# Kernel tuning notes

Measured on AMD Instinct MI355X. Metric: run time of the kernel, lower is better.

## Reference

```python
import jax, jax.numpy as jnp
import numpy as np


def _hungarian(cost):
    """Jonker-Volgenant shortest-augmenting-path LAP solver (minimum cost).

    Returns col_ind such that rows arange(n) are matched to columns col_ind,
    identical (in objective) to scipy.optimize.linear_sum_assignment.
    Runs on host numpy, mirroring the original's detach().cpu() + scipy path.
    """
    cost = np.asarray(cost, dtype=np.float64)
    n = cost.shape[0]
    INF = np.inf
    u = np.zeros(n + 1)
    v = np.zeros(n + 1)
    p = np.zeros(n + 1, dtype=np.int64)   # p[j]: row (1-based) assigned to column j
    way = np.zeros(n + 1, dtype=np.int64)
    for i in range(1, n + 1):
        p[0] = i
        j0 = 0
        minv = np.full(n + 1, INF)
        used = np.zeros(n + 1, dtype=bool)
        while True:
            used[j0] = True
            i0 = p[j0]
            # vectorized relaxation of reduced costs for all unused columns
            cur = cost[i0 - 1] - u[i0] - v[1:]
            free = ~used[1:]
            upd = free & (cur < minv[1:])
            minv[1:] = np.where(upd, cur, minv[1:])
            way[1:] = np.where(upd, j0, way[1:])
            cand = np.where(free, minv[1:], INF)
            j1 = int(np.argmin(cand)) + 1
            delta = cand[j1 - 1]
            u[p[used]] += delta
            v[used] -= delta
            minv[1:] = np.where(free, minv[1:] - delta, minv[1:])
            j0 = j1
            if p[j0] == 0:
                break
        # augment along the alternating path
        while j0:
            j1 = way[j0]
            p[j0] = p[j1]
            j0 = j1
    col = np.empty(n, dtype=np.int64)
    col[p[1:] - 1] = np.arange(n)
    return col


def setup_inputs() -> dict:
    key = jax.random.key(0)
    B, N = 64, 256
    D = jax.random.normal(key, (B, N, N), dtype=jnp.float32)
    return {"D": D}


def reference(D):
    # Host round-trip for the assignment, exactly as the torch module does
    # (D.detach().cpu().numpy() -> scipy LAP per batch element).
    Dn = np.asarray(jax.device_get(D))
    cols = np.stack([_hungarian(Dn[b]) for b in range(Dn.shape[0])])  # [B, N]
    idx = jnp.asarray(cols)[:, :, None]                               # [B, N, 1]
    # gather matched costs D[b, i, col[b, i]] and reduce: mean per batch, then mean
    matched = jnp.take_along_axis(D, idx, axis=2)[..., 0]             # [B, N]
    return matched.mean(axis=1).mean()
```

## Files before the change

### kernel.cpp

```cpp
#include <hip/hip_runtime.h>

#define N_DIM 256
#define BATCH 64
#define BS 64
#define SCALE 4096.0f

#define DPP_MINU(x, ctrl) do {                                                 \
    unsigned _s = (unsigned)__builtin_amdgcn_update_dpp((int)(x), (int)(x),    \
                                                        (ctrl), 0xf, 0xf, false); \
    (x) = ((x) < _s) ? (x) : _s;                                               \
} while (0)

__device__ __forceinline__ unsigned wave_min_u32(unsigned x) {
    DPP_MINU(x, 0x111);
    DPP_MINU(x, 0x112);
    DPP_MINU(x, 0x114);
    DPP_MINU(x, 0x118);
    const unsigned a = (unsigned)__builtin_amdgcn_readlane((int)x, 15);
    const unsigned b = (unsigned)__builtin_amdgcn_readlane((int)x, 31);
    const unsigned c = (unsigned)__builtin_amdgcn_readlane((int)x, 47);
    const unsigned d = (unsigned)__builtin_amdgcn_readlane((int)x, 63);
    const unsigned ab = (a < b) ? a : b;
    const unsigned cd = (c < d) ? c : d;
    return (ab < cd) ? ab : cd;
}

__device__ __forceinline__ int rd4_i(int x0, int x1, int x2, int x3, int idx) {
    const int sel = idx & 3, src = idx >> 2;
    int ab = (sel & 1) ? x1 : x0;
    int cd = (sel & 1) ? x3 : x2;
    int vv = (sel & 2) ? cd : ab;
    return __builtin_amdgcn_readlane(vv, src);
}

#define SET4(x0, x1, x2, x3, idx, val) do {                                    \
    const int _sel = (idx) & 3;                                                \
    if (t == ((idx) >> 2)) {                                                   \
        if (_sel == 0) x0 = (val); else if (_sel == 1) x1 = (val);             \
        else if (_sel == 2) x2 = (val); else x3 = (val);                       \
    }                                                                          \
} while (0)

__device__ __forceinline__ int lo16(int p) { return (int)(short)(p & 0xFFFF); }
__device__ __forceinline__ int hi16(int p) { return p >> 16; }

__global__ __launch_bounds__(BS) void lap_kernel(const float* __restrict__ Dm,
                                                 double* __restrict__ batch_sums) {
    const int b = blockIdx.x;
    const int t = threadIdx.x;
    const float* __restrict__ cost = Dm + (size_t)b * N_DIM * N_DIM;
    const float4* __restrict__ cost4 = (const float4*)cost;

    __shared__ int2     chi[N_DIM * BS];
    __shared__ int      u_s[N_DIM];
    __shared__ int      v_s[N_DIM];
    __shared__ int      row4col_s[N_DIM];
    __shared__ int      col4row_s[N_DIM];
    __shared__ int      queue_s[N_DIM];
    __shared__ unsigned bid_s[N_DIM];
    __shared__ int      qcnt_s;

    const int c0i = 4 * t, c1i = 4 * t + 1, c2i = 4 * t + 2, c3i = 4 * t + 3;

    int cmn0 = INT_MAX, cmn1 = INT_MAX, cmn2 = INT_MAX, cmn3 = INT_MAX;
    int ca0 = 0, ca1 = 0, ca2 = 0, ca3 = 0;
    for (int r = 0; r < N_DIM; ++r) {
        const float4 c4 = cost4[r * BS + t];
        const int a0 = __float2int_rn(c4.x * SCALE);
        const int a1 = __float2int_rn(c4.y * SCALE);
        const int a2 = __float2int_rn(c4.z * SCALE);
        const int a3 = __float2int_rn(c4.w * SCALE);
        int2 p;
        p.x = (a0 & 0xFFFF) | (a1 << 16);
        p.y = (a2 & 0xFFFF) | (a3 << 16);
        chi[r * BS + t] = p;
        if (a0 < cmn0) { cmn0 = a0; ca0 = r; }
        if (a1 < cmn1) { cmn1 = a1; ca1 = r; }
        if (a2 < cmn2) { cmn2 = a2; ca2 = r; }
        if (a3 < cmn3) { cmn3 = a3; ca3 = r; }
    }
    {
        int4 vv; vv.x = cmn0; vv.y = cmn1; vv.z = cmn2; vv.w = cmn3;
        ((int4*)v_s)[t] = vv;
        int4 zz; zz.x = 0; zz.y = 0; zz.z = 0; zz.w = 0;
        ((int4*)u_s)[t] = zz;
        int4 mm; mm.x = -1; mm.y = -1; mm.z = -1; mm.w = -1;
        ((int4*)row4col_s)[t] = mm;
        ((int4*)col4row_s)[t] = mm;
        int4 rc; rc.x = 0x7fffffff; rc.y = 0x7fffffff; rc.z = 0x7fffffff; rc.w = 0x7fffffff;
        ((int4*)queue_s)[t] = rc;
        uint4 bb; bb.x = ~0u; bb.y = ~0u; bb.z = ~0u; bb.w = ~0u;
        ((uint4*)bid_s)[t] = bb;
    }
    __syncthreads();
    atomicMin(&queue_s[ca0], c0i);
    atomicMin(&queue_s[ca1], c1i);
    atomicMin(&queue_s[ca2], c2i);
    atomicMin(&queue_s[ca3], c3i);
    __syncthreads();
    if (queue_s[ca0] == c0i) { row4col_s[c0i] = ca0; col4row_s[ca0] = c0i; }
    if (queue_s[ca1] == c1i) { row4col_s[c1i] = ca1; col4row_s[ca1] = c1i; }
    if (queue_s[ca2] == c2i) { row4col_s[c2i] = ca2; col4row_s[ca2] = c2i; }
    if (queue_s[ca3] == c3i) { row4col_s[c3i] = ca3; col4row_s[ca3] = c3i; }
    __syncthreads();

    for (int pass = 0; pass < 64; ++pass) {
        if (t == 0) qcnt_s = 0;
        __syncthreads();
        {
            const int4 my = ((const int4*)col4row_s)[t];
            const int nf = (my.x < 0) + (my.y < 0) + (my.z < 0) + (my.w < 0);
            if (nf) {
                int pos = atomicAdd(&qcnt_s, nf);
                if (my.x < 0) queue_s[pos++] = c0i;
                if (my.y < 0) queue_s[pos++] = c1i;
                if (my.z < 0) queue_s[pos++] = c2i;
                if (my.w < 0) queue_s[pos++] = c3i;
            }
        }
        __syncthreads();
        const int n = qcnt_s;
        if (n == 0) break;
        for (int base = 0; base < n; base += BS) {
            const int my_row = (base + t < n) ? queue_s[base + t] : -1;
            int d1 = INT_MAX, d2 = INT_MAX;
            int j1 = 0;
            if (my_row >= 0) {
                const int rb = my_row * BS;
                for (int l = 0; l < BS; ++l) {
                    const int l2 = (l + t) & 63;
                    const int2 h = chi[rb + l2];
                    const int4 vv = ((const int4*)v_s)[l2];
                    int d;
                    d = lo16(h.x) - vv.x; if (d < d1) { d2 = d1; d1 = d; j1 = 4 * l2 + 0; } else if (d < d2) d2 = d;
                    d = hi16(h.x) - vv.y; if (d < d1) { d2 = d1; d1 = d; j1 = 4 * l2 + 1; } else if (d < d2) d2 = d;
                    d = lo16(h.y) - vv.z; if (d < d1) { d2 = d1; d1 = d; j1 = 4 * l2 + 2; } else if (d < d2) d2 = d;
                    d = hi16(h.y) - vv.w; if (d < d1) { d2 = d1; d1 = d; j1 = 4 * l2 + 3; } else if (d < d2) d2 = d;
                }
                atomicMin(&bid_s[j1], ((unsigned)d1 << 8) | (unsigned)t);
            }
            __syncthreads();
            if (my_row >= 0) {
                const unsigned mybid = ((unsigned)d1 << 8) | (unsigned)t;
                if (bid_s[j1] == mybid) {
                    const int i0 = row4col_s[j1];
                    row4col_s[j1] = my_row;
                    col4row_s[my_row] = j1;
                    if (i0 >= 0) col4row_s[i0] = -1;
                    u_s[my_row] = d2;
                    v_s[j1] += d1 - d2 - 1;
                    bid_s[j1] = ~0u;
                }
            }
            __syncthreads();
        }
    }

    const int4 vv4 = ((const int4*)v_s)[t];
    int vn0 = -vv4.x, vn1 = -vv4.y, vn2 = -vv4.z, vn3 = -vv4.w;
    const int4 m4 = ((const int4*)row4col_s)[t];
    int r4c0 = m4.x, r4c1 = m4.y, r4c2 = m4.z, r4c3 = m4.w;
    const int4 y4 = ((const int4*)col4row_s)[t];
    int c4r0 = y4.x, c4r1 = y4.y, c4r2 = y4.z, c4r3 = y4.w;
    int p0 = 0, p1 = 0, p2 = 0, p3 = 0;

    unsigned long long fm0 = __ballot(c4r0 < 0);
    unsigned long long fm1 = __ballot(c4r1 < 0);
    unsigned long long fm2 = __ballot(c4r2 < 0);
    unsigned long long fm3 = __ballot(c4r3 < 0);

    const int KINIT0 = (0x7FFFFF << 8) | c0i;
    const int KINIT1 = (0x7FFFFF << 8) | c1i;
    const int KINIT2 = (0x7FFFFF << 8) | c2i;
    const int KINIT3 = (0x7FFFFF << 8) | c3i;

    while (fm0 | fm1 | fm2 | fm3) {
        int i;
        if (fm0)      { const int tt = __builtin_ctzll(fm0); fm0 &= fm0 - 1; i = tt * 4 + 0; }
        else if (fm1) { const int tt = __builtin_ctzll(fm1); fm1 &= fm1 - 1; i = tt * 4 + 1; }
        else if (fm2) { const int tt = __builtin_ctzll(fm2); fm2 &= fm2 - 1; i = tt * 4 + 2; }
        else          { const int tt = __builtin_ctzll(fm3); fm3 &= fm3 - 1; i = tt * 4 + 3; }

        int k0 = KINIT0, k1 = KINIT1, k2 = KINIT2, k3 = KINIT3;
        int g0 = 0, g1 = 0, g2 = 0, g3 = 0;
        int cur = i;
        int minVal = 0;
        int sink = -1;

        while (true) {
            const int2 h   = chi[cur * BS + t];
            const int ucur = u_s[cur];
            const int add  = minVal - ucur;

            int r, kn;
            r  = add + lo16(h.x) + vn0;
            kn = (r << 8) | c0i; if (kn < k0) { p0 = cur; k0 = kn; }
            r  = add + hi16(h.x) + vn1;
            kn = (r << 8) | c1i; if (kn < k1) { p1 = cur; k1 = kn; }
            r  = add + lo16(h.y) + vn2;
            kn = (r << 8) | c2i; if (kn < k2) { p2 = cur; k2 = kn; }
            r  = add + hi16(h.y) + vn3;
            kn = (r << 8) | c3i; if (kn < k3) { p3 = cur; k3 = kn; }

            const int q0 = k0 | g0, q1 = k1 | g1, q2 = k2 | g2, q3 = k3 | g3;
            int q01 = (q0 < q1) ? q0 : q1;
            int q23 = (q2 < q3) ? q2 : q3;
            const int gk = (int)wave_min_u32((unsigned)((q01 < q23) ? q01 : q23));

            const int bi = gk & 0xFF;
            minVal = gk >> 8;
            const int r4 = rd4_i(r4c0, r4c1, r4c2, r4c3, bi);
            if (t == (bi >> 2)) {
                const int s = bi & 3;
                if (s == 0) g0 = 0x7FFFFFFF; else if (s == 1) g1 = 0x7FFFFFFF;
                else if (s == 2) g2 = 0x7FFFFFFF; else g3 = 0x7FFFFFFF;
            }
            if (r4 < 0) { sink = bi; break; }
            cur = r4;
        }

        if (g0) { const int dv = minVal - (k0 >> 8); vn0 += dv; if (r4c0 >= 0) u_s[r4c0] += dv; }
        if (g1) { const int dv = minVal - (k1 >> 8); vn1 += dv; if (r4c1 >= 0) u_s[r4c1] += dv; }
        if (g2) { const int dv = minVal - (k2 >> 8); vn2 += dv; if (r4c2 >= 0) u_s[r4c2] += dv; }
        if (g3) { const int dv = minVal - (k3 >> 8); vn3 += dv; if (r4c3 >= 0) u_s[r4c3] += dv; }
        if (t == 0) u_s[i] += minVal;

        if (sink >= 0) {
            int jj = sink;
            while (true) {
                const int ii = rd4_i(p0, p1, p2, p3, jj);
                SET4(r4c0, r4c1, r4c2, r4c3, jj, ii);
                const int tmp = rd4_i(c4r0, c4r1, c4r2, c4r3, ii);
                SET4(c4r0, c4r1, c4r2, c4r3, ii, jj);
                jj = tmp;
                if (ii == i) break;
            }
        }
    }

    double s = 0.0;
    s += (double)cost[(size_t)(t * 4 + 0) * N_DIM + c4r0];
    s += (double)cost[(size_t)(t * 4 + 1) * N_DIM + c4r1];
    s += (double)cost[(size_t)(t * 4 + 2) * N_DIM + c4r2];
    s += (double)cost[(size_t)(t * 4 + 3) * N_DIM + c4r3];
    #pragma unroll
    for (int off = 32; off > 0; off >>= 1) s += __shfl_down(s, off);
    if (t == 0) batch_sums[b] = s;
}

__global__ void finalize_kernel(const double* __restrict__ batch_sums,
                                float* __restrict__ out) {
    const int t = threadIdx.x;
    double s = batch_sums[t];
    #pragma unroll
    for (int off = 32; off > 0; off >>= 1) s += __shfl_down(s, off);
    if (t == 0) out[0] = (float)(s / (double)((long long)BATCH * N_DIM));
}

extern "C" void kernel_launch(void* const* d_in, const int* in_sizes, int n_in,
                              void* d_out, int out_size, void* d_ws, size_t ws_size,
                              hipStream_t stream) {
    const float* Dm = (const float*)d_in[0];
    float* out = (float*)d_out;
    double* sums = (double*)d_ws;

    lap_kernel<<<BATCH, BS, 0, stream>>>(Dm, sums);
    finalize_kernel<<<1, 64, 0, stream>>>(sums, out);
}
```

Measured before the change: 825.0 us.

## Replace fixed-epsilon auction passes with epsilon-scaling phases and eps-feasibility pruning

```diff
diff --git a/kernel.cpp b/kernel.cpp
--- a/kernel.cpp
+++ b/kernel.cpp
@@ -4,6 +4,7 @@
 #define BATCH 64
 #define BS 64
 #define SCALE 4096.0f
+#define NPHASE 5
 
 #define DPP_MINU(x, ctrl) do {                                                 \
     unsigned _s = (unsigned)__builtin_amdgcn_update_dpp((int)(x), (int)(x),    \
@@ -43,6 +44,12 @@
 
 __device__ __forceinline__ int lo16(int p) { return (int)(short)(p & 0xFFFF); }
 __device__ __forceinline__ int hi16(int p) { return p >> 16; }
+
+__device__ __forceinline__ int chi_at(const int2* chi, int row, int col) {
+    const int2 w = chi[row * BS + (col >> 2)];
+    const int word = (col & 2) ? w.y : w.x;
+    return (col & 1) ? hi16(word) : lo16(word);
+}
 
 __global__ __launch_bounds__(BS) void lap_kernel(const float* __restrict__ Dm,
                                                  double* __restrict__ batch_sums) {
@@ -89,8 +96,6 @@
         ((int4*)col4row_s)[t] = mm;
         int4 rc; rc.x = 0x7fffffff; rc.y = 0x7fffffff; rc.z = 0x7fffffff; rc.w = 0x7fffffff;
         ((int4*)queue_s)[t] = rc;
-        uint4 bb; bb.x = ~0u; bb.y = ~0u; bb.z = ~0u; bb.w = ~0u;
-        ((uint4*)bid_s)[t] = bb;
     }
     __syncthreads();
     atomicMin(&queue_s[ca0], c0i);
@@ -104,56 +109,100 @@
     if (queue_s[ca3] == c3i) { row4col_s[c3i] = ca3; col4row_s[ca3] = c3i; }
     __syncthreads();
 
-    for (int pass = 0; pass < 64; ++pass) {
-        if (t == 0) qcnt_s = 0;
-        __syncthreads();
-        {
-            const int4 my = ((const int4*)col4row_s)[t];
-            const int nf = (my.x < 0) + (my.y < 0) + (my.z < 0) + (my.w < 0);
-            if (nf) {
-                int pos = atomicAdd(&qcnt_s, nf);
-                if (my.x < 0) queue_s[pos++] = c0i;
-                if (my.y < 0) queue_s[pos++] = c1i;
-                if (my.z < 0) queue_s[pos++] = c2i;
-                if (my.w < 0) queue_s[pos++] = c3i;
-            }
-        }
-        __syncthreads();
-        const int n = qcnt_s;
-        if (n == 0) break;
-        for (int base = 0; base < n; base += BS) {
-            const int my_row = (base + t < n) ? queue_s[base + t] : -1;
-            int d1 = INT_MAX, d2 = INT_MAX;
-            int j1 = 0;
-            if (my_row >= 0) {
-                const int rb = my_row * BS;
-                for (int l = 0; l < BS; ++l) {
-                    const int l2 = (l + t) & 63;
-                    const int2 h = chi[rb + l2];
-                    const int4 vv = ((const int4*)v_s)[l2];
-                    int d;
-                    d = lo16(h.x) - vv.x; if (d < d1) { d2 = d1; d1 = d; j1 = 4 * l2 + 0; } else if (d < d2) d2 = d;
-                    d = hi16(h.x) - vv.y; if (d < d1) { d2 = d1; d1 = d; j1 = 4 * l2 + 1; } else if (d < d2) d2 = d;
-                    d = lo16(h.y) - vv.z; if (d < d1) { d2 = d1; d1 = d; j1 = 4 * l2 + 2; } else if (d < d2) d2 = d;
-                    d = hi16(h.y) - vv.w; if (d < d1) { d2 = d1; d1 = d; j1 = 4 * l2 + 3; } else if (d < d2) d2 = d;
-                }
-                atomicMin(&bid_s[j1], ((unsigned)d1 << 8) | (unsigned)t);
-            }
+    const int eps_tab[NPHASE] = {2048, 256, 32, 4, 1};
+    const int cap_tab[NPHASE] = {10, 10, 12, 14, 18};
+    for (int ph = 0; ph < NPHASE; ++ph) {
+        const int eps = eps_tab[ph];
+        for (int pass = 0; pass < cap_tab[ph]; ++pass) {
+            if (t == 0) qcnt_s = 0;
             __syncthreads();
-            if (my_row >= 0) {
-                const unsigned mybid = ((unsigned)d1 << 8) | (unsigned)t;
-                if (bid_s[j1] == mybid) {
-                    const int i0 = row4col_s[j1];
-                    row4col_s[j1] = my_row;
-                    col4row_s[my_row] = j1;
-                    if (i0 >= 0) col4row_s[i0] = -1;
-                    u_s[my_row] = d2;
-                    v_s[j1] += d1 - d2 - 1;
-                    bid_s[j1] = ~0u;
+            {
+                uint4 bb; bb.x = ~0u; bb.y = ~0u; bb.z = ~0u; bb.w = ~0u;
+                ((uint4*)bid_s)[t] = bb;
+                const int4 my = ((const int4*)col4row_s)[t];
+                const int nf = (my.x < 0) + (my.y < 0) + (my.z < 0) + (my.w < 0);
+                if (nf) {
+                    int pos = atomicAdd(&qcnt_s, nf);
+                    if (my.x < 0) queue_s[pos++] = c0i;
+                    if (my.y < 0) queue_s[pos++] = c1i;
+                    if (my.z < 0) queue_s[pos++] = c2i;
+                    if (my.w < 0) queue_s[pos++] = c3i;
                 }
             }
             __syncthreads();
-        }
+            const int n = qcnt_s;
+            if (n == 0) break;
+            for (int base = 0; base < n; base += BS) {
+                const int my_row = (base + t < n) ? queue_s[base + t] : -1;
+                int d1 = INT_MAX, d2 = INT_MAX;
+                int j1 = 0;
+                if (my_row >= 0) {
+                    const int rb = my_row * BS;
+                    for (int l = 0; l < BS; ++l) {
+                        const int l2 = (l + t) & 63;
+                        const int2 h = chi[rb + l2];
+                        const int4 vv = ((const int4*)v_s)[l2];
+                        int d;
+                        d = lo16(h.x) - vv.x; if (d < d1) { d2 = d1; d1 = d; j1 = 4 * l2 + 0; } else if (d < d2) d2 = d;
+                        d = hi16(h.x) - vv.y; if (d < d1) { d2 = d1; d1 = d; j1 = 4 * l2 + 1; } else if (d < d2) d2 = d;
+                        d = lo16(h.y) - vv.z; if (d < d1) { d2 = d1; d1 = d; j1 = 4 * l2 + 2; } else if (d < d2) d2 = d;
+                        d = hi16(h.y) - vv.w; if (d < d1) { d2 = d1; d1 = d; j1 = 4 * l2 + 3; } else if (d < d2) d2 = d;
+                    }
+                    atomicMin(&bid_s[j1], ((unsigned)d1 << 8) | (unsigned)t);
+                }
+                __syncthreads();
+                if (my_row >= 0) {
+                    const unsigned mybid = ((unsigned)d1 << 8) | (unsigned)t;
+                    if (bid_s[j1] == mybid) {
+                        const int i0 = row4col_s[j1];
+                        row4col_s[j1] = my_row;
+                        col4row_s[my_row] = j1;
+                        if (i0 >= 0) col4row_s[i0] = -1;
+                        v_s[j1] += d1 - d2 - eps;
+                    }
+                }
+                __syncthreads();
+            }
+        }
+
+        int m0 = INT_MAX, m1 = INT_MAX, m2 = INT_MAX, m3 = INT_MAX;
+        for (int l = 0; l < BS; ++l) {
+            const int l2 = (l + t) & 63;
+            const int4 vv = ((const int4*)v_s)[l2];
+            const int2 h0 = chi[c0i * BS + l2];
+            const int2 h1 = chi[c1i * BS + l2];
+            const int2 h2 = chi[c2i * BS + l2];
+            const int2 h3 = chi[c3i * BS + l2];
+            int d;
+            d = lo16(h0.x) - vv.x; if (d < m0) m0 = d;
+            d = hi16(h0.x) - vv.y; if (d < m0) m0 = d;
+            d = lo16(h0.y) - vv.z; if (d < m0) m0 = d;
+            d = hi16(h0.y) - vv.w; if (d < m0) m0 = d;
+            d = lo16(h1.x) - vv.x; if (d < m1) m1 = d;
+            d = hi16(h1.x) - vv.y; if (d < m1) m1 = d;
+            d = lo16(h1.y) - vv.z; if (d < m1) m1 = d;
+            d = hi16(h1.y) - vv.w; if (d < m1) m1 = d;
+            d = lo16(h2.x) - vv.x; if (d < m2) m2 = d;
+            d = hi16(h2.x) - vv.y; if (d < m2) m2 = d;
+            d = lo16(h2.y) - vv.z; if (d < m2) m2 = d;
+            d = hi16(h2.y) - vv.w; if (d < m2) m2 = d;
+            d = lo16(h3.x) - vv.x; if (d < m3) m3 = d;
+            d = hi16(h3.x) - vv.y; if (d < m3) m3 = d;
+            d = lo16(h3.y) - vv.z; if (d < m3) m3 = d;
+            d = hi16(h3.y) - vv.w; if (d < m3) m3 = d;
+        }
+        const bool last = (ph == NPHASE - 1);
+        const int thr = last ? 0 : eps_tab[ph + 1];
+        const int4 my = ((const int4*)col4row_s)[t];
+        if (my.x >= 0 && chi_at(chi, c0i, my.x) - v_s[my.x] - m0 > thr) { col4row_s[c0i] = -1; row4col_s[my.x] = -1; }
+        if (my.y >= 0 && chi_at(chi, c1i, my.y) - v_s[my.y] - m1 > thr) { col4row_s[c1i] = -1; row4col_s[my.y] = -1; }
+        if (my.z >= 0 && chi_at(chi, c2i, my.z) - v_s[my.z] - m2 > thr) { col4row_s[c2i] = -1; row4col_s[my.z] = -1; }
+        if (my.w >= 0 && chi_at(chi, c3i, my.w) - v_s[my.w] - m3 > thr) { col4row_s[c3i] = -1; row4col_s[my.w] = -1; }
+        if (last) {
+            int4 uu; uu.x = m0; uu.y = m1; uu.z = m2; uu.w = m3;
+            ((int4*)u_s)[t] = uu;
+        }
+        __syncthreads();
     }
 
     const int4 vv4 = ((const int4*)v_s)[t];
```

Result: slower. 988.3 us (+19.8%).
